# Performance work log

Measured on AMD Instinct MI355X. Metric: run time of the kernel, lower is better.

Reference implementation:

```python
import jax, jax.numpy as jnp
import numpy as np

B, T, F, D, H, L = 4, 1024, 128, 512, 8, 4
DFF = 4 * D
NE, MD = 16, 20
HD = D // H
SCALE = 1.0 / HD ** 0.5


def _ln(x, w, b):
    m = jnp.mean(x, axis=-1, keepdims=True)
    v = jnp.mean((x - m) ** 2, axis=-1, keepdims=True)
    return (x - m) * jax.lax.rsqrt(v + 1e-5) * w + b


def setup_inputs() -> dict:
    key = jax.random.key(0)
    ks = jax.random.split(key, 16)
    rn = lambda k, shape: jax.random.normal(k, shape, jnp.float32) * 0.02
    return {
        'node_features': jax.random.normal(ks[0], (B, T, F), jnp.float32),
        'centrality': jax.random.uniform(ks[1], (B, T), jnp.float32),
        'edge_types': jax.random.randint(ks[2], (B, T, T), 0, NE),
        'sp_dist': jax.random.randint(ks[3], (B, T, T), 0, MD + 1),
        'node_W': rn(ks[4], (F, D)), 'node_b': jnp.zeros((D,), jnp.float32),
        'cent_W': rn(ks[5], (D,)), 'cent_b': jnp.zeros((D,), jnp.float32),
        'edge_emb': rn(ks[6], (NE, H)), 'dist_emb': rn(ks[7], (MD + 1, H)),
        'ln1_w': jnp.ones((L, D), jnp.float32), 'ln1_b': jnp.zeros((L, D), jnp.float32),
        'q_W': rn(ks[8], (L, D, D)), 'q_b': jnp.zeros((L, D), jnp.float32),
        'k_W': rn(ks[9], (L, D, D)), 'k_b': jnp.zeros((L, D), jnp.float32),
        'v_W': rn(ks[10], (L, D, D)), 'v_b': jnp.zeros((L, D), jnp.float32),
        'o_W': rn(ks[11], (L, D, D)), 'o_b': jnp.zeros((L, D), jnp.float32),
        'ln2_w': jnp.ones((L, D), jnp.float32), 'ln2_b': jnp.zeros((L, D), jnp.float32),
        'f1_W': rn(ks[12], (L, D, DFF)), 'f1_b': jnp.zeros((L, DFF), jnp.float32),
        'f2_W': rn(ks[13], (L, DFF, D)), 'f2_b': jnp.zeros((L, D), jnp.float32),
    }


def _forward(node_features, centrality, edge_types, sp_dist,
             node_W, node_b, cent_W, cent_b, edge_emb, dist_emb,
             ln1_w, ln1_b, q_W, q_b, k_W, k_b, v_W, v_b, o_W, o_b,
             ln2_w, ln2_b, f1_W, f1_b, f2_W, f2_b):
    # node embedding + centrality encoding
    h = node_features @ node_W + node_b                      # [B,T,D]
    h = h + centrality[..., None] * cent_W + cent_b          # Linear(1,D)
    # Graphormer attention bias: [B,T,T,H] -> [B,H,T,T]
    sp = jnp.clip(sp_dist, 0, MD)
    attn_bias = (edge_emb[edge_types] + dist_emb[sp]).transpose(0, 3, 1, 2)

    def step(h, p):
        l1w, l1b, qW, qb, kW, kb, vW, vb, oW, ob, l2w, l2b, w1, b1, w2, b2 = p
        x = _ln(h, l1w, l1b)
        q = (x @ qW + qb).reshape(B, T, H, HD)
        k = (x @ kW + kb).reshape(B, T, H, HD)
        v = (x @ vW + vb).reshape(B, T, H, HD)
        scores = jnp.einsum('bihd,bjhd->bhij', q, k) * SCALE + attn_bias
        attn = jax.nn.softmax(scores, axis=-1)
        o = jnp.einsum('bhij,bjhd->bihd', attn, v).reshape(B, T, D)
        h = h + (o @ oW + ob)                                # dropout in eval mode
        x2 = _ln(h, l2w, l2b)
        h = h + (jax.nn.silu(x2 @ w1 + b1) @ w2 + b2)
        return h, None

    layer_params = (ln1_w, ln1_b, q_W, q_b, k_W, k_b, v_W, v_b, o_W, o_b,
                    ln2_w, ln2_b, f1_W, f1_b, f2_W, f2_b)
    h, _ = jax.lax.scan(step, h, layer_params)
    return h


def reference(node_features, centrality, edge_types, sp_dist,
              node_W, node_b, cent_W, cent_b, edge_emb, dist_emb,
              ln1_w, ln1_b, q_W, q_b, k_W, k_b, v_W, v_b, o_W, o_b,
              ln2_w, ln2_b, f1_W, f1_b, f2_W, f2_b):
    return _forward(node_features, centrality, edge_types, sp_dist,
                    node_W, node_b, cent_W, cent_b, edge_emb, dist_emb,
                    ln1_w, ln1_b, q_W, q_b, k_W, k_b, v_W, v_b, o_W, o_b,
                    ln2_w, ln2_b, f1_W, f1_b, f2_W, f2_b)
```

## Files before the change

### kernel.cpp

```cpp
#include <hip/hip_runtime.h>
#include <cstddef>
#include <cstdint>

#define B_    4
#define T_    1024
#define F_    128
#define D_    512
#define H_    8
#define L_    4
#define DFF_  2048
#define HD_   64
#define SCALE_ 0.125f
#define LOG2E_ 1.4426950408889634f
#define CL2E_  (SCALE_ * LOG2E_)

typedef __attribute__((ext_vector_type(8))) short bf16x8;
typedef __attribute__((ext_vector_type(4))) float f32x4;

#define AS1(p) ((const __attribute__((address_space(1))) void*)(p))
#define AS3(p) ((__attribute__((address_space(3))) void*)(p))

__device__ __forceinline__ short f2bf(float f) {
    unsigned u = __float_as_uint(f);
    u += 0x7FFFu + ((u >> 16) & 1u);
    return (short)(u >> 16);
}
__device__ __forceinline__ float bf2f(short s) {
    return __uint_as_float(((unsigned)(unsigned short)s) << 16);
}

#define PIPE_BARRIER(rem, W2, W1)                                             \
    if ((rem) >= 2)      asm volatile("s_waitcnt vmcnt(" #W2 ")" ::: "memory"); \
    else if ((rem) == 1) asm volatile("s_waitcnt vmcnt(" #W1 ")" ::: "memory"); \
    else                 asm volatile("s_waitcnt vmcnt(0)"      ::: "memory"); \
    __builtin_amdgcn_s_barrier();                                             \
    __builtin_amdgcn_sched_barrier(0);

template <int NP>
__global__ __launch_bounds__(256) void ln_k(
    float* __restrict__ X, const float* __restrict__ P0,
    const float* __restrict__ P1, const float* __restrict__ w,
    const float* __restrict__ b, short* __restrict__ Y)
{
    const int row = blockIdx.x;
    const int tid = threadIdx.x;
    float* xr = X + (size_t)row * D_;
    float v0 = xr[tid];
    float v1 = xr[tid + 256];
    if (NP == 2) {
        const size_t o0 = (size_t)row * D_ + tid;
        const size_t o1 = o0 + 256;
        v0 += P0[o0] + P1[o0];
        v1 += P0[o1] + P1[o1];
        xr[tid]       = v0;
        xr[tid + 256] = v1;
    }
    float s  = v0 + v1;
    float s2 = v0 * v0 + v1 * v1;
#pragma unroll
    for (int off = 1; off < 64; off <<= 1) {
        s  += __shfl_xor(s,  off);
        s2 += __shfl_xor(s2, off);
    }
    __shared__ float ss[4], ss2[4];
    if ((tid & 63) == 0) { ss[tid >> 6] = s; ss2[tid >> 6] = s2; }
    __syncthreads();
    s  = ss[0]  + ss[1]  + ss[2]  + ss[3];
    s2 = ss2[0] + ss2[1] + ss2[2] + ss2[3];
    const float mean = s * (1.f / D_);
    const float var  = s2 * (1.f / D_) - mean * mean;
    const float r    = rsqrtf(var + 1e-5f);
    short* yr = Y + (size_t)row * D_;
    yr[tid]       = f2bf((v0 - mean) * r * w[tid]       + b[tid]);
    yr[tid + 256] = f2bf((v1 - mean) * r * w[tid + 256] + b[tid + 256]);
}

__global__ __launch_bounds__(256) void red_k(
    const float* __restrict__ X, const float* __restrict__ P0,
    const float* __restrict__ P1, float* __restrict__ Dst)
{
    const int i = (blockIdx.x * 256 + threadIdx.x) << 2;
    const float4 a = *(const float4*)(X + i);
    const float4 p = *(const float4*)(P0 + i);
    const float4 q = *(const float4*)(P1 + i);
    *(float4*)(Dst + i) = make_float4(a.x + p.x + q.x, a.y + p.y + q.y,
                                      a.z + p.z + q.z, a.w + p.w + q.w);
}

__global__ __launch_bounds__(256) void setup_k(
    const float* __restrict__ qW, const float* __restrict__ kW,
    const float* __restrict__ vW, const float* __restrict__ oW,
    const float* __restrict__ f1W, const float* __restrict__ f2W,
    const float* __restrict__ nW,
    short* __restrict__ WqkvT, short* __restrict__ WoT,
    short* __restrict__ Wf1T, short* __restrict__ Wf2T,
    short* __restrict__ nWt,
    const int* __restrict__ et, const int* __restrict__ sp,
    const float* __restrict__ ee, const float* __restrict__ de,
    unsigned char* __restrict__ biasT8,
    const float* __restrict__ nf, short* __restrict__ nfb,
    const float* __restrict__ qb, const float* __restrict__ kb,
    const float* __restrict__ vb, float* __restrict__ biasf)
{
    const int bid = blockIdx.x;
    const int tid = threadIdx.x;

    if (bid < 12352) {
        const float* src; short* dst; int K, N, nt, tile;
        if (bid < 3072) {
            const int mat = bid >> 8;  tile = bid & 255;
            const int l = mat / 3, which = mat % 3;
            const float* s3 = (which == 0) ? qW : (which == 1) ? kW : vW;
            src = s3 + (size_t)l * D_ * D_;
            dst = WqkvT + (size_t)mat * D_ * D_;
            K = D_; N = D_; nt = 16;
        } else if (bid < 4096) {
            const int mat = (bid - 3072) >> 8;  tile = (bid - 3072) & 255;
            src = oW + (size_t)mat * D_ * D_;  dst = WoT + (size_t)mat * D_ * D_;
            K = D_; N = D_; nt = 16;
        } else if (bid < 8192) {
            const int mat = (bid - 4096) >> 10; tile = (bid - 4096) & 1023;
            src = f1W + (size_t)mat * D_ * DFF_; dst = Wf1T + (size_t)mat * DFF_ * D_;
            K = D_; N = DFF_; nt = 64;
        } else if (bid < 12288) {
            const int mat = (bid - 8192) >> 10; tile = (bid - 8192) & 1023;
            src = f2W + (size_t)mat * DFF_ * D_; dst = Wf2T + (size_t)mat * D_ * DFF_;
            K = DFF_; N = D_; nt = 16;
        } else {
            tile = bid - 12288;
            src = nW; dst = nWt; K = F_; N = D_; nt = 16;
        }
        const int k0 = (tile / nt) << 5, n0 = (tile % nt) << 5;
        __shared__ float t[32][33];
        const int c = tid & 31, r0 = tid >> 5;
#pragma unroll
        for (int i = 0; i < 32; i += 8)
            t[r0 + i][c] = src[(size_t)(k0 + r0 + i) * N + n0 + c];
        __syncthreads();
#pragma unroll
        for (int i = 0; i < 32; i += 8)
            dst[(size_t)(n0 + r0 + i) * K + k0 + c] = f2bf(t[c][r0 + i]);
        return;
    }

    const int pb = bid - 12352;
    if (pb >= 4096) {
        if (pb < 4608) {
            const int i = (((pb - 4096) << 8) + tid) << 2;
            const float4 v = *(const float4*)(nf + i);
            *(short4*)(nfb + i) =
                make_short4(f2bf(v.x), f2bf(v.y), f2bf(v.z), f2bf(v.w));
        } else {
            const int i = ((pb - 4608) << 8) + tid;
            const int l = i / 1536, c = i % 1536;
            float v;
            if (c < 512)       v = qb[l * 512 + c];
            else if (c < 1024) v = kb[l * 512 + c - 512];
            else               v = vb[l * 512 + c - 1024];
            biasf[i] = v;
        }
        return;
    }
    __shared__ float eeS[16][9], deS[21][9];
    if (tid < 128) eeS[tid >> 3][tid & 7] = ee[tid];
    for (int t2 = tid; t2 < 168; t2 += 256)
        deS[t2 >> 3][t2 & 7] = de[t2];
    __syncthreads();
    const int gid = pb * 256 + tid;
    const int j4  = (gid & 255) << 2;
    const int bi  = gid >> 8;
    const size_t base = (size_t)bi * T_ + j4;
    const int4 e = *(const int4*)(et + base);
    const int4 s = *(const int4*)(sp + base);
    const int b = bi >> 10, i = bi & 1023;
    const int ex[4] = {e.x, e.y, e.z, e.w};
    const int sx[4] = {min(s.x, 20), min(s.y, 20), min(s.z, 20), min(s.w, 20)};
#pragma unroll
    for (int h = 0; h < 8; ++h) {
        uchar4 o;
        float v;
        v = (eeS[ex[0]][h] + deS[sx[0]][h]) * LOG2E_ + 0.5f;
        o.x = (unsigned char)(int)fminf(fmaxf(v * 255.f + 0.5f, 0.f), 255.f);
        v = (eeS[ex[1]][h] + deS[sx[1]][h]) * LOG2E_ + 0.5f;
        o.y = (unsigned char)(int)fminf(fmaxf(v * 255.f + 0.5f, 0.f), 255.f);
        v = (eeS[ex[2]][h] + deS[sx[2]][h]) * LOG2E_ + 0.5f;
        o.z = (unsigned char)(int)fminf(fmaxf(v * 255.f + 0.5f, 0.f), 255.f);
        v = (eeS[ex[3]][h] + deS[sx[3]][h]) * LOG2E_ + 0.5f;
        o.w = (unsigned char)(int)fminf(fmaxf(v * 255.f + 0.5f, 0.f), 255.f);
        *(uchar4*)(biasT8 + ((size_t)((b * H_ + h) * T_ + i)) * T_ + j4) = o;
    }
}

__global__ __launch_bounds__(256) void embed_mm_k(
    const short* __restrict__ A, const short* __restrict__ Wt,
    const float* __restrict__ nb, const float* __restrict__ cb,
    const float* __restrict__ cW, const float* __restrict__ cent,
    float* __restrict__ C)
{
    const int K = F_, N = D_;
    __shared__ short As[4][128 * 32];
    __shared__ short Bs[4][64 * 32];
    const int tid  = threadIdx.x;
    const int lane = tid & 63, wv = tid >> 6;
    const int lb = blockIdx.x;
    const int xcd = lb & 7, jj = lb >> 3;
    const int bx = jj & 7, by = (xcd << 2) + (jj >> 3);
    const int bm = by << 7, bn = bx << 6;
    const int wm = (wv & 1) << 6, wn = (wv >> 1) << 5;

    const int c0 = (wv << 6) + lane;
    const int m0 = c0 >> 2, q0 = (c0 & 3) ^ ((m0 >> 1) & 3);
    const int c1 = 256 + c0;
    const int m1 = c1 >> 2, q1 = (c1 & 3) ^ ((m1 >> 1) & 3);

    const short* gA0 = A  + (size_t)(bm + m0) * K + (q0 << 3);
    const short* gA1 = A  + (size_t)(bm + m1) * K + (q1 << 3);
    const short* gB0 = Wt + (size_t)(bn + m0) * K + (q0 << 3);

    f32x4 acc[4][2];
#pragma unroll
    for (int i = 0; i < 4; ++i)
#pragma unroll
        for (int j = 0; j < 2; ++j)
            acc[i][j] = (f32x4){0.f, 0.f, 0.f, 0.f};

    const int fm = lane & 15, fq = lane >> 4;
    int caddr[4], baddr[2];
#pragma unroll
    for (int t = 0; t < 4; ++t) {
        const int rowA = wm + (t << 4) + fm;
        caddr[t] = ((rowA << 2) + (fq ^ ((rowA >> 1) & 3))) << 3;
    }
#pragma unroll
    for (int t = 0; t < 2; ++t) {
        const int rowB = wn + (t << 4) + fm;
        baddr[t] = ((rowB << 2) + (fq ^ ((rowB >> 1) & 3))) << 3;
    }

#define EMB_STAGE(KK, BUF) do { \
    __builtin_amdgcn_global_load_lds(AS1(gA0 + (KK)), AS3(&As[BUF][(wv << 9)]),        16, 0, 0); \
    __builtin_amdgcn_global_load_lds(AS1(gA1 + (KK)), AS3(&As[BUF][2048 + (wv << 9)]), 16, 0, 0); \
    __builtin_amdgcn_global_load_lds(AS1(gB0 + (KK)), AS3(&Bs[BUF][(wv << 9)]),        16, 0, 0); \
} while (0)

    EMB_STAGE(0, 0); EMB_STAGE(32, 1); EMB_STAGE(64, 2);
    const int nt = K >> 5;
    for (int t = 0; t < nt; ++t) {
        const int rem = nt - 1 - t;
        PIPE_BARRIER(rem, 6, 3);
        if (rem >= 3) EMB_STAGE((t + 3) << 5, (t + 3) & 3);
        const short* Asc = As[t & 3];
        const short* Bsc = Bs[t & 3];
        bf16x8 af[4], bf[2];
#pragma unroll
        for (int u = 0; u < 4; ++u) af[u] = *(const bf16x8*)(Asc + caddr[u]);
#pragma unroll
        for (int u = 0; u < 2; ++u) bf[u] = *(const bf16x8*)(Bsc + baddr[u]);
#pragma unroll
        for (int i = 0; i < 4; ++i)
#pragma unroll
            for (int j = 0; j < 2; ++j)
                acc[i][j] = __builtin_amdgcn_mfma_f32_16x16x32_bf16(
                    af[i], bf[j], acc[i][j], 0, 0, 0);
    }
#undef EMB_STAGE

    const int col0 = bn + wn + fm;
    const int row0 = bm + wm + (fq << 2);
#pragma unroll
    for (int j = 0; j < 2; ++j) {
        const int colg = col0 + (j << 4);
        const float bb = nb[colg] + cb[colg];
        const float cw = cW[colg];
#pragma unroll
        for (int i = 0; i < 4; ++i) {
#pragma unroll
            for (int r = 0; r < 4; ++r) {
                const int rowg = row0 + (i << 4) + r;
                C[(size_t)rowg * N + colg] = acc[i][j][r] + bb + cent[rowg] * cw;
            }
        }
    }
}

template <int OUTM, int ACT, int RES>
__global__ __launch_bounds__(256) void mm_k(
    const short* __restrict__ A, const short* __restrict__ Wt,
    const float* __restrict__ bias, const float* __restrict__ R,
    void* __restrict__ Cv, int M, int N, int K)
{
    __shared__ short As[4][128 * 32];
    __shared__ short Bs[4][128 * 32];
    const int tid  = threadIdx.x;
    const int lane = tid & 63, wv = tid >> 6;
    const int lb = blockIdx.x;
    const int xcd = lb & 7, jj = lb >> 3;
    const int bx = jj & 15, by = (xcd << 2) + (jj >> 4);
    const int bm = by << 7, bn = bx << 7;
    const int wm = (wv & 1) << 6, wn = (wv >> 1) << 6;

    const int c0 = (wv << 6) + lane;
    const int m0 = c0 >> 2, q0 = (c0 & 3) ^ ((m0 >> 1) & 3);
    const int c1 = 256 + c0;
    const int m1 = c1 >> 2, q1 = (c1 & 3) ^ ((m1 >> 1) & 3);

    const short* gA0 = A  + (size_t)(bm + m0) * K + (q0 << 3);
    const short* gA1 = A  + (size_t)(bm + m1) * K + (q1 << 3);
    const short* gB0 = Wt + (size_t)(bn + m0) * K + (q0 << 3);
    const short* gB1 = Wt + (size_t)(bn + m1) * K + (q1 << 3);

    f32x4 acc[4][4];
#pragma unroll
    for (int i = 0; i < 4; ++i)
#pragma unroll
        for (int j = 0; j < 4; ++j)
            acc[i][j] = (f32x4){0.f, 0.f, 0.f, 0.f};

    const int fm = lane & 15, fq = lane >> 4;
    int caddr[4], baddr[4];
#pragma unroll
    for (int t = 0; t < 4; ++t) {
        const int rowA = wm + (t << 4) + fm;
        caddr[t] = ((rowA << 2) + (fq ^ ((rowA >> 1) & 3))) << 3;
        const int rowB = wn + (t << 4) + fm;
        baddr[t] = ((rowB << 2) + (fq ^ ((rowB >> 1) & 3))) << 3;
    }

#define MM_STAGE(KK, BUF) do { \
    __builtin_amdgcn_global_load_lds(AS1(gA0 + (KK)), AS3(&As[BUF][(wv << 9)]),        16, 0, 0); \
    __builtin_amdgcn_global_load_lds(AS1(gA1 + (KK)), AS3(&As[BUF][2048 + (wv << 9)]), 16, 0, 0); \
    __builtin_amdgcn_global_load_lds(AS1(gB0 + (KK)), AS3(&Bs[BUF][(wv << 9)]),        16, 0, 0); \
    __builtin_amdgcn_global_load_lds(AS1(gB1 + (KK)), AS3(&Bs[BUF][2048 + (wv << 9)]), 16, 0, 0); \
} while (0)

    MM_STAGE(0, 0); MM_STAGE(32, 1); MM_STAGE(64, 2);
    const int nt = K >> 5;
    for (int t = 0; t < nt; ++t) {
        const int rem = nt - 1 - t;
        PIPE_BARRIER(rem, 8, 4);
        if (rem >= 3) MM_STAGE((t + 3) << 5, (t + 3) & 3);
        const short* Asc = As[t & 3];
        const short* Bsc = Bs[t & 3];
        bf16x8 af[4], bf[4];
#pragma unroll
        for (int u = 0; u < 4; ++u) {
            af[u] = *(const bf16x8*)(Asc + caddr[u]);
            bf[u] = *(const bf16x8*)(Bsc + baddr[u]);
        }
#pragma unroll
        for (int i = 0; i < 4; ++i)
#pragma unroll
            for (int j = 0; j < 4; ++j)
                acc[i][j] = __builtin_amdgcn_mfma_f32_16x16x32_bf16(
                    af[i], bf[j], acc[i][j], 0, 0, 0);
    }
#undef MM_STAGE

    const int col0 = bn + wn + fm;
    const int row0 = bm + wm + (fq << 2);
    float* Cf = (float*)Cv;
    short* Cb = (short*)Cv;
#pragma unroll
    for (int j = 0; j < 4; ++j) {
        const int colg = col0 + (j << 4);
        const float bb = bias[colg];
#pragma unroll
        for (int i = 0; i < 4; ++i) {
#pragma unroll
            for (int r = 0; r < 4; ++r) {
                const int rowg = row0 + (i << 4) + r;
                float v = acc[i][j][r] + bb;
                if (ACT) v = v / (1.f + __expf(-v));
                const size_t off = (size_t)rowg * N + colg;
                if (RES) v += R[off];
                if (OUTM == 1) Cb[off] = f2bf(v);
                else           Cf[off] = v;
            }
        }
    }
}

__global__ __launch_bounds__(256) void qkv64_k(
    const short* __restrict__ A, const short* __restrict__ Wt,
    const float* __restrict__ bias, short* __restrict__ QKb,
    short* __restrict__ VtOut)
{
    const int K = D_;
    __shared__ short As[4][128 * 32];
    __shared__ short Bs[4][64 * 32];
    const int tid  = threadIdx.x;
    const int lane = tid & 63, wv = tid >> 6;
    const int lb = blockIdx.x;
    const int xcd = lb & 7, jj = lb >> 3;
    const int yl = jj / 24, bx = jj - yl * 24;
    const int by = (xcd << 2) + yl;
    const int bm = by << 7, bn = bx << 6;
    const int wm = (wv & 1) << 6, wn = (wv >> 1) << 5;

    const int c0 = (wv << 6) + lane;
    const int m0 = c0 >> 2, q0 = (c0 & 3) ^ ((m0 >> 1) & 3);
    const int c1 = 256 + c0;
    const int m1 = c1 >> 2, q1 = (c1 & 3) ^ ((m1 >> 1) & 3);

    const short* gA0 = A  + (size_t)(bm + m0) * K + (q0 << 3);
    const short* gA1 = A  + (size_t)(bm + m1) * K + (q1 << 3);
    const short* gB0 = Wt + (size_t)(bn + m0) * K + (q0 << 3);

    f32x4 acc[4][2];
#pragma unroll
    for (int i = 0; i < 4; ++i)
#pragma unroll
        for (int j = 0; j < 2; ++j)
            acc[i][j] = (f32x4){0.f, 0.f, 0.f, 0.f};

    const int fm = lane & 15, fq = lane >> 4;
    int caddr[4], baddr[2];
#pragma unroll
    for (int t = 0; t < 4; ++t) {
        const int rowA = wm + (t << 4) + fm;
        caddr[t] = ((rowA << 2) + (fq ^ ((rowA >> 1) & 3))) << 3;
    }
#pragma unroll
    for (int t = 0; t < 2; ++t) {
        const int rowB = wn + (t << 4) + fm;
        baddr[t] = ((rowB << 2) + (fq ^ ((rowB >> 1) & 3))) << 3;
    }

#define QKV_STAGE(KK, BUF) do { \
    __builtin_amdgcn_global_load_lds(AS1(gA0 + (KK)), AS3(&As[BUF][(wv << 9)]),        16, 0, 0); \
    __builtin_amdgcn_global_load_lds(AS1(gA1 + (KK)), AS3(&As[BUF][2048 + (wv << 9)]), 16, 0, 0); \
    __builtin_amdgcn_global_load_lds(AS1(gB0 + (KK)), AS3(&Bs[BUF][(wv << 9)]),        16, 0, 0); \
} while (0)

    QKV_STAGE(0, 0); QKV_STAGE(32, 1); QKV_STAGE(64, 2);
    const int nt = K >> 5;
    for (int t = 0; t < nt; ++t) {
        const int rem = nt - 1 - t;
        PIPE_BARRIER(rem, 6, 3);
        if (rem >= 3) QKV_STAGE((t + 3) << 5, (t + 3) & 3);
        const short* Asc = As[t & 3];
        const short* Bsc = Bs[t & 3];
        bf16x8 af[4], bf[2];
#pragma unroll
        for (int u = 0; u < 4; ++u) af[u] = *(const bf16x8*)(Asc + caddr[u]);
#pragma unroll
        for (int u = 0; u < 2; ++u) bf[u] = *(const bf16x8*)(Bsc + baddr[u]);
#pragma unroll
        for (int i = 0; i < 4; ++i)
#pragma unroll
            for (int j = 0; j < 2; ++j)
                acc[i][j] = __builtin_amdgcn_mfma_f32_16x16x32_bf16(
                    af[i], bf[j], acc[i][j], 0, 0, 0);
    }
#undef QKV_STAGE

    const int col0 = bn + wn + fm;
    const int row0 = bm + wm + (fq << 2);
#pragma unroll
    for (int j = 0; j < 2; ++j) {
        const int colg = col0 + (j << 4);
        const float bb = bias[colg];
#pragma unroll
        for (int i = 0; i < 4; ++i) {
#pragma unroll
            for (int r = 0; r < 4; ++r) {
                const int rowg = row0 + (i << 4) + r;
                const float v = acc[i][j][r] + bb;
                if (colg < 1024) {
                    QKb[(size_t)rowg * 1024 + colg] = f2bf(v);
                } else {
                    const int da = colg - 1024;
                    const int hh = da >> 6, dd = da & 63;
                    const int bb2 = rowg >> 10, tt = rowg & 1023;
                    VtOut[((size_t)(bb2 * H_ + hh) * 64 + dd) * T_ + tt] = f2bf(v);
                }
            }
        }
    }
}

__global__ __launch_bounds__(256) void flash_k(
    const short* __restrict__ QKb, const short* __restrict__ Vt,
    const unsigned char* __restrict__ biasT8, short* __restrict__ OpartB,
    float* __restrict__ Lpart)
{
    const int tid = threadIdx.x;
    const int bx = blockIdx.x;
    const int it = bx >> 1, split = bx & 1;
    const int i0 = it << 6;
    const int h  = blockIdx.y;
    const int b  = blockIdx.z;
    const int lane = tid & 63, w = tid >> 6;
    const int fm = lane & 15, q = lane >> 4;

    __shared__ short Ks[4096];
    __shared__ short Vs[4096];
    __shared__ unsigned char Bsh8[4096];
    __shared__ short Ps[64][72];

    const short* qp = QKb + (size_t)(b * T_ + i0 + (w << 4) + fm) * 1024 + (h << 6) + (q << 3);
    const bf16x8 aq0 = *(const bf16x8*)(qp);
    const bf16x8 aq1 = *(const bf16x8*)(qp + 32);

    const int s0 = (w << 6) + lane, r0 = s0 >> 3, cc0 = (s0 & 7) ^ (r0 & 7);
    const int s1 = 256 + s0,        r1 = s1 >> 3, cc1 = (s1 & 7) ^ (r1 & 7);
    const short* gK0 = QKb + (size_t)(b * T_ + r0) * 1024 + 512 + (h << 6) + (cc0 << 3);
    const short* gK1 = QKb + (size_t)(b * T_ + r1) * 1024 + 512 + (h << 6) + (cc1 << 3);
    const short* gV0 = Vt + ((size_t)((b * H_ + h) << 6) + r0) * T_ + (cc0 << 3);
    const short* gV1 = Vt + ((size_t)((b * H_ + h) << 6) + r1) * T_ + (cc1 << 3);
    const int br = s0 >> 2, bc = (s0 & 3) ^ (br & 3);
    const unsigned char* gB0 = biasT8 +
        ((size_t)(b * H_ + h) * T_ + i0 + br) * T_ + (bc << 4);

    int fAddr[4][2];
#pragma unroll
    for (int t = 0; t < 4; ++t) {
        const int row = (t << 4) + fm;
#pragma unroll
        for (int ks = 0; ks < 2; ++ks)
            fAddr[t][ks] = (row << 6) + (((q + (ks << 2)) ^ (row & 7)) << 3);
    }

    int bAddr[4][4];
#pragma unroll
    for (int r = 0; r < 4; ++r) {
        const int rowL = (w << 4) + (q << 2) + r;
#pragma unroll
        for (int jt = 0; jt < 4; ++jt)
            bAddr[r][jt] = (rowL << 6) + (((jt ^ (rowL & 3))) << 4) + fm;
    }

    const short oneb = 0x3F80;
    const bf16x8 ones = {oneb, oneb, oneb, oneb, oneb, oneb, oneb, oneb};

    f32x4 accO[4];
#pragma unroll
    for (int dt = 0; dt < 4; ++dt) accO[dt] = (f32x4){0.f, 0.f, 0.f, 0.f};
    f32x4 accL = (f32x4){0.f, 0.f, 0.f, 0.f};

    const int irow = b * T_ + i0 + (w << 4) + (q << 2);
    short* psW = &Ps[(w << 4) + (q << 2)][fm];
    const short* psR = &Ps[(w << 4) + fm][q << 3];

    const int jbeg = split << 9, jend = jbeg + 512;
    for (int j0 = jbeg; j0 < jend; j0 += 64) {
        __syncthreads();
        __builtin_amdgcn_global_load_lds(AS1(gK0 + (size_t)j0 * 1024), AS3(Ks + (s0 << 3)), 16, 0, 0);
        __builtin_amdgcn_global_load_lds(AS1(gK1 + (size_t)j0 * 1024), AS3(Ks + (s1 << 3)), 16, 0, 0);
        __builtin_amdgcn_global_load_lds(AS1(gV0 + j0), AS3(Vs + (s0 << 3)), 16, 0, 0);
        __builtin_amdgcn_global_load_lds(AS1(gV1 + j0), AS3(Vs + (s1 << 3)), 16, 0, 0);
        __builtin_amdgcn_global_load_lds(AS1(gB0 + j0), AS3(Bsh8 + (s0 << 4)), 16, 0, 0);
        __syncthreads();

        f32x4 s[4];
#pragma unroll
        for (int jt = 0; jt < 4; ++jt) s[jt] = (f32x4){0.f, 0.f, 0.f, 0.f};
        __builtin_amdgcn_s_setprio(1);
#pragma unroll
        for (int jt = 0; jt < 4; ++jt) {
            const bf16x8 k0 = *(const bf16x8*)(Ks + fAddr[jt][0]);
            const bf16x8 k1 = *(const bf16x8*)(Ks + fAddr[jt][1]);
            s[jt] = __builtin_amdgcn_mfma_f32_16x16x32_bf16(aq0, k0, s[jt], 0, 0, 0);
            s[jt] = __builtin_amdgcn_mfma_f32_16x16x32_bf16(aq1, k1, s[jt], 0, 0, 0);
        }
        __builtin_amdgcn_s_setprio(0);

#pragma unroll
        for (int r = 0; r < 4; ++r)
#pragma unroll
            for (int jt = 0; jt < 4; ++jt) {
                const float q8 = (float)Bsh8[bAddr[r][jt]];
                const float bb = fmaf(q8, 1.f / 255.f, -0.5f);
                const float p = __builtin_amdgcn_exp2f(fmaf(s[jt][r], CL2E_, bb));
                psW[(size_t)r * 72 + (jt << 4)] = f2bf(p);
            }

        __builtin_amdgcn_s_setprio(1);
#pragma unroll
        for (int ks = 0; ks < 2; ++ks) {
            const bf16x8 ap = *(const bf16x8*)(psR + (ks << 5));
            accL = __builtin_amdgcn_mfma_f32_16x16x32_bf16(ap, ones, accL, 0, 0, 0);
#pragma unroll
            for (int dt = 0; dt < 4; ++dt) {
                const bf16x8 bv = *(const bf16x8*)(Vs + fAddr[dt][ks]);
                accO[dt] = __builtin_amdgcn_mfma_f32_16x16x32_bf16(ap, bv, accO[dt], 0, 0, 0);
            }
        }
        __builtin_amdgcn_s_setprio(0);
    }

    short* obase = OpartB + (size_t)split * B_ * T_ * D_;
#pragma unroll
    for (int r = 0; r < 4; ++r) {
        short* op = obase + (size_t)(irow + r) * D_ + (h << 6) + fm;
#pragma unroll
        for (int dt = 0; dt < 4; ++dt)
            op[dt << 4] = f2bf(accO[dt][r]);
    }
    if (fm == 0) {
#pragma unroll
        for (int r = 0; r < 4; ++r)
            Lpart[(size_t)split * B_ * T_ * H_ + (size_t)(irow + r) * H_ + h] = accL[r];
    }
}

__global__ __launch_bounds__(256) void combine_k(
    const short* __restrict__ OpartB, const float* __restrict__ Lpart,
    short* __restrict__ Ob)
{
    const int gid = blockIdx.x * 256 + threadIdx.x;
    const int d4  = (gid & 127) << 2;
    const int row = gid >> 7;
    const int h   = d4 >> 6;
    const float l = Lpart[(size_t)row * H_ + h] +
                    Lpart[(size_t)B_ * T_ * H_ + (size_t)row * H_ + h];
    const float inv = 1.f / l;
    const size_t o = (size_t)row * D_ + d4;
    const short4 a = *(const short4*)(OpartB + o);
    const short4 c = *(const short4*)(OpartB + (size_t)B_ * T_ * D_ + o);
    short4 r = make_short4(
        f2bf((bf2f(a.x) + bf2f(c.x)) * inv), f2bf((bf2f(a.y) + bf2f(c.y)) * inv),
        f2bf((bf2f(a.z) + bf2f(c.z)) * inv), f2bf((bf2f(a.w) + bf2f(c.w)) * inv));
    *(short4*)(Ob + o) = r;
}

__global__ __launch_bounds__(256) void mm64p_k(
    const short* __restrict__ A, const short* __restrict__ Wt,
    const float* __restrict__ bias, float* __restrict__ P,
    int M, int N, int K, int KS)
{
    __shared__ short As[4][128 * 32];
    __shared__ short Bs[4][64 * 32];
    const int tid  = threadIdx.x;
    const int lane = tid & 63, wv = tid >> 6;
    const int lb = blockIdx.x;
    const int xcd = lb & 7, jj = lb >> 3;
    const int z  = jj >> 5;
    const int jr = jj & 31;
    const int bx = jr & 7, by = (xcd << 2) + (jr >> 3);
    const int bm = by << 7, bn = bx << 6;
    const int ks0 = z * KS;
    const int wm = (wv & 1) << 6, wn = (wv >> 1) << 5;

    const int c0 = (wv << 6) + lane;
    const int m0 = c0 >> 2, q0 = (c0 & 3) ^ ((m0 >> 1) & 3);
    const int c1 = 256 + c0;
    const int m1 = c1 >> 2, q1 = (c1 & 3) ^ ((m1 >> 1) & 3);

    const short* gA0 = A  + (size_t)(bm + m0) * K + ks0 + (q0 << 3);
    const short* gA1 = A  + (size_t)(bm + m1) * K + ks0 + (q1 << 3);
    const short* gB0 = Wt + (size_t)(bn + m0) * K + ks0 + (q0 << 3);

    f32x4 acc[4][2];
#pragma unroll
    for (int i = 0; i < 4; ++i)
#pragma unroll
        for (int j = 0; j < 2; ++j)
            acc[i][j] = (f32x4){0.f, 0.f, 0.f, 0.f};

    const int fm = lane & 15, fq = lane >> 4;
    int caddr[4], baddr[2];
#pragma unroll
    for (int t = 0; t < 4; ++t) {
        const int rowA = wm + (t << 4) + fm;
        caddr[t] = ((rowA << 2) + (fq ^ ((rowA >> 1) & 3))) << 3;
    }
#pragma unroll
    for (int t = 0; t < 2; ++t) {
        const int rowB = wn + (t << 4) + fm;
        baddr[t] = ((rowB << 2) + (fq ^ ((rowB >> 1) & 3))) << 3;
    }

#define MM64_STAGE(KK, BUF) do { \
    __builtin_amdgcn_global_load_lds(AS1(gA0 + (KK)), AS3(&As[BUF][(wv << 9)]),        16, 0, 0); \
    __builtin_amdgcn_global_load_lds(AS1(gA1 + (KK)), AS3(&As[BUF][2048 + (wv << 9)]), 16, 0, 0); \
    __builtin_amdgcn_global_load_lds(AS1(gB0 + (KK)), AS3(&Bs[BUF][(wv << 9)]),        16, 0, 0); \
} while (0)

    MM64_STAGE(0, 0); MM64_STAGE(32, 1); MM64_STAGE(64, 2);
    const int nt = KS >> 5;
    for (int t = 0; t < nt; ++t) {
        const int rem = nt - 1 - t;
        PIPE_BARRIER(rem, 6, 3);
        if (rem >= 3) MM64_STAGE((t + 3) << 5, (t + 3) & 3);
        const short* Asc = As[t & 3];
        const short* Bsc = Bs[t & 3];
        bf16x8 af[4], bf[2];
#pragma unroll
        for (int u = 0; u < 4; ++u) af[u] = *(const bf16x8*)(Asc + caddr[u]);
#pragma unroll
        for (int u = 0; u < 2; ++u) bf[u] = *(const bf16x8*)(Bsc + baddr[u]);
#pragma unroll
        for (int i = 0; i < 4; ++i)
#pragma unroll
            for (int j = 0; j < 2; ++j)
                acc[i][j] = __builtin_amdgcn_mfma_f32_16x16x32_bf16(
                    af[i], bf[j], acc[i][j], 0, 0, 0);
    }
#undef MM64_STAGE

    const int col0 = bn + wn + fm;
    const int row0 = bm + wm + (fq << 2);
    float* Pz = P + (size_t)z * M * N;
#pragma unroll
    for (int j = 0; j < 2; ++j) {
        const int colg = col0 + (j << 4);
        const float bb = (z == 0) ? bias[colg] : 0.f;
#pragma unroll
        for (int i = 0; i < 4; ++i) {
#pragma unroll
            for (int r = 0; r < 4; ++r) {
                const int rowg = row0 + (i << 4) + r;
                Pz[(size_t)rowg * N + colg] = acc[i][j][r] + bb;
            }
        }
    }
}

extern "C" void kernel_launch(void* const* d_in, const int* in_sizes, int n_in,
                              void* d_out, int out_size, void* d_ws, size_t ws_size,
                              hipStream_t stream)
{
    (void)in_sizes; (void)n_in; (void)out_size; (void)ws_size;

    const float* nf   = (const float*)d_in[0];
    const float* cent = (const float*)d_in[1];
    const int*   et   = (const int*)  d_in[2];
    const int*   sp   = (const int*)  d_in[3];
    const float* nW   = (const float*)d_in[4];
    const float* nb   = (const float*)d_in[5];
    const float* cW   = (const float*)d_in[6];
    const float* cb   = (const float*)d_in[7];
    const float* ee   = (const float*)d_in[8];
    const float* de   = (const float*)d_in[9];
    const float* ln1w = (const float*)d_in[10];
    const float* ln1b = (const float*)d_in[11];
    const float* qW   = (const float*)d_in[12];
    const float* qb   = (const float*)d_in[13];
    const float* kW   = (const float*)d_in[14];
    const float* kb   = (const float*)d_in[15];
    const float* vW   = (const float*)d_in[16];
    const float* vb   = (const float*)d_in[17];
    const float* oW   = (const float*)d_in[18];
    const float* ob   = (const float*)d_in[19];
    const float* ln2w = (const float*)d_in[20];
    const float* ln2b = (const float*)d_in[21];
    const float* f1W  = (const float*)d_in[22];
    const float* f1b  = (const float*)d_in[23];
    const float* f2W  = (const float*)d_in[24];
    const float* f2b  = (const float*)d_in[25];

    const int M = B_ * T_;
    char* p = (char*)d_ws;
    float* Hbuf  = (float*)p;  p += (size_t)M * D_ * 4;
    short* QKb   = (short*)p;  p += (size_t)M * 1024 * 2;
    short* Vt    = (short*)p;  p += (size_t)B_ * H_ * 64 * T_ * 2;
    float* biasf = (float*)p;  p += (size_t)L_ * 3 * D_ * 4;
    short* Xbuf  = (short*)p;  p += (size_t)M * D_ * 2;
    short* Ob    = (short*)p;  p += (size_t)M * D_ * 2;
    short* FF    = (short*)p;  p += (size_t)M * DFF_ * 2;
    unsigned char* biasT8 = (unsigned char*)p; p += (size_t)B_ * H_ * T_ * T_;
    short* WqkvT = (short*)p;  p += (size_t)L_ * 3 * D_ * D_ * 2;
    short* WoT   = (short*)p;  p += (size_t)L_ * D_ * D_ * 2;
    short* Wf1T  = (short*)p;  p += (size_t)L_ * DFF_ * D_ * 2;
    short* Wf2T  = (short*)p;  p += (size_t)L_ * D_ * DFF_ * 2;
    short* nfb   = (short*)p;  p += (size_t)M * F_ * 2;
    short* nWt   = (short*)p;  p += (size_t)D_ * F_ * 2;
    short* OpartB = (short*)p; p += (size_t)2 * M * D_ * 2;
    float* Lpart = (float*)p;  p += (size_t)2 * M * H_ * 4;
    float* Pbuf  = (float*)p;  p += (size_t)2 * M * D_ * 4;

    float* out = (float*)d_out;

    setup_k<<<dim3(16984), dim3(256), 0, stream>>>(
        qW, kW, vW, oW, f1W, f2W, nW, WqkvT, WoT, Wf1T, Wf2T, nWt,
        et, sp, ee, de, biasT8, nf, nfb, qb, kb, vb, biasf);
    embed_mm_k<<<dim3(256), dim3(256), 0, stream>>>(
        nfb, nWt, nb, cb, cW, cent, Hbuf);

    const dim3 blk(256);
    const dim3 gQKV(768);
    const dim3 gO64p(512);
    const dim3 gF1 (512);
    const dim3 gAttn(2 * T_ / 64, H_, B_);
    const dim3 gCmb(M * D_ / 1024);

    for (int l = 0; l < L_; ++l) {
        const size_t bOff  = (size_t)l * D_;
        const size_t b1Off = (size_t)l * DFF_;

        if (l == 0)
            ln_k<0><<<dim3(M), blk, 0, stream>>>(
                Hbuf, nullptr, nullptr, ln1w + bOff, ln1b + bOff, Xbuf);
        else
            ln_k<2><<<dim3(M), blk, 0, stream>>>(
                Hbuf, Pbuf, Pbuf + (size_t)M * D_, ln1w + bOff, ln1b + bOff, Xbuf);

        qkv64_k<<<gQKV, blk, 0, stream>>>(
            Xbuf, WqkvT + (size_t)l * 3 * D_ * D_, biasf + (size_t)l * 3 * D_,
            QKb, Vt);

        flash_k<<<gAttn, blk, 0, stream>>>(QKb, Vt, biasT8, OpartB, Lpart);
        combine_k<<<gCmb, blk, 0, stream>>>(OpartB, Lpart, Ob);

        mm64p_k<<<gO64p, blk, 0, stream>>>(
            Ob, WoT + (size_t)l * D_ * D_, ob + bOff, Pbuf, M, D_, D_, D_ / 2);

        ln_k<2><<<dim3(M), blk, 0, stream>>>(
            Hbuf, Pbuf, Pbuf + (size_t)M * D_, ln2w + bOff, ln2b + bOff, Xbuf);

        mm_k<1, 1, 0><<<gF1, blk, 0, stream>>>(
            Xbuf, Wf1T + (size_t)l * DFF_ * D_, f1b + b1Off, nullptr, FF, M, DFF_, D_);

        mm64p_k<<<gO64p, blk, 0, stream>>>(
            FF, Wf2T + (size_t)l * D_ * DFF_, f2b + bOff, Pbuf, M, D_, DFF_, DFF_ / 2);
    }

    red_k<<<gCmb, blk, 0, stream>>>(Hbuf, Pbuf, Pbuf + (size_t)M * D_, out);
}
```

Measured before the change: 633.6 us.

## Drop split-KV in flash attention and normalize output in-kernel, removing combine pass

The attention kernel no longer splits the key range into two halves. Each block now loops over all 1024 keys and writes the normalized output directly, so the combine kernel and its partial-output and partial-sum buffers are gone. This removes one launch per layer and the round trip of the partial results through memory, at the cost of half as many attention blocks (512 instead of 1024) and a longer serial loop per block. The s_setprio hints around the MFMA sections are also removed.

```diff
diff --git a/kernel.cpp b/kernel.cpp
--- a/kernel.cpp
+++ b/kernel.cpp
@@ -481,13 +481,10 @@
 
 __global__ __launch_bounds__(256) void flash_k(
     const short* __restrict__ QKb, const short* __restrict__ Vt,
-    const unsigned char* __restrict__ biasT8, short* __restrict__ OpartB,
-    float* __restrict__ Lpart)
+    const unsigned char* __restrict__ biasT8, short* __restrict__ Ob)
 {
     const int tid = threadIdx.x;
-    const int bx = blockIdx.x;
-    const int it = bx >> 1, split = bx & 1;
-    const int i0 = it << 6;
+    const int i0 = blockIdx.x << 6;
     const int h  = blockIdx.y;
     const int b  = blockIdx.z;
     const int lane = tid & 63, w = tid >> 6;
@@ -542,8 +539,7 @@
     short* psW = &Ps[(w << 4) + (q << 2)][fm];
     const short* psR = &Ps[(w << 4) + fm][q << 3];
 
-    const int jbeg = split << 9, jend = jbeg + 512;
-    for (int j0 = jbeg; j0 < jend; j0 += 64) {
+    for (int j0 = 0; j0 < T_; j0 += 64) {
         __syncthreads();
         __builtin_amdgcn_global_load_lds(AS1(gK0 + (size_t)j0 * 1024), AS3(Ks + (s0 << 3)), 16, 0, 0);
         __builtin_amdgcn_global_load_lds(AS1(gK1 + (size_t)j0 * 1024), AS3(Ks + (s1 << 3)), 16, 0, 0);
@@ -555,7 +551,6 @@
         f32x4 s[4];
 #pragma unroll
         for (int jt = 0; jt < 4; ++jt) s[jt] = (f32x4){0.f, 0.f, 0.f, 0.f};
-        __builtin_amdgcn_s_setprio(1);
 #pragma unroll
         for (int jt = 0; jt < 4; ++jt) {
             const bf16x8 k0 = *(const bf16x8*)(Ks + fAddr[jt][0]);
@@ -563,7 +558,6 @@
             s[jt] = __builtin_amdgcn_mfma_f32_16x16x32_bf16(aq0, k0, s[jt], 0, 0, 0);
             s[jt] = __builtin_amdgcn_mfma_f32_16x16x32_bf16(aq1, k1, s[jt], 0, 0, 0);
         }
-        __builtin_amdgcn_s_setprio(0);
 
 #pragma unroll
         for (int r = 0; r < 4; ++r)
@@ -575,7 +569,6 @@
                 psW[(size_t)r * 72 + (jt << 4)] = f2bf(p);
             }
 
-        __builtin_amdgcn_s_setprio(1);
 #pragma unroll
         for (int ks = 0; ks < 2; ++ks) {
             const bf16x8 ap = *(const bf16x8*)(psR + (ks << 5));
@@ -586,42 +579,16 @@
                 accO[dt] = __builtin_amdgcn_mfma_f32_16x16x32_bf16(ap, bv, accO[dt], 0, 0, 0);
             }
         }
-        __builtin_amdgcn_s_setprio(0);
-    }
-
-    short* obase = OpartB + (size_t)split * B_ * T_ * D_;
+    }
+
 #pragma unroll
     for (int r = 0; r < 4; ++r) {
-        short* op = obase + (size_t)(irow + r) * D_ + (h << 6) + fm;
+        const float inv = 1.f / accL[r];
+        short* op = Ob + (size_t)(irow + r) * D_ + (h << 6) + fm;
 #pragma unroll
         for (int dt = 0; dt < 4; ++dt)
-            op[dt << 4] = f2bf(accO[dt][r]);
-    }
-    if (fm == 0) {
-#pragma unroll
-        for (int r = 0; r < 4; ++r)
-            Lpart[(size_t)split * B_ * T_ * H_ + (size_t)(irow + r) * H_ + h] = accL[r];
-    }
-}
-
-__global__ __launch_bounds__(256) void combine_k(
-    const short* __restrict__ OpartB, const float* __restrict__ Lpart,
-    short* __restrict__ Ob)
-{
-    const int gid = blockIdx.x * 256 + threadIdx.x;
-    const int d4  = (gid & 127) << 2;
-    const int row = gid >> 7;
-    const int h   = d4 >> 6;
-    const float l = Lpart[(size_t)row * H_ + h] +
-                    Lpart[(size_t)B_ * T_ * H_ + (size_t)row * H_ + h];
-    const float inv = 1.f / l;
-    const size_t o = (size_t)row * D_ + d4;
-    const short4 a = *(const short4*)(OpartB + o);
-    const short4 c = *(const short4*)(OpartB + (size_t)B_ * T_ * D_ + o);
-    short4 r = make_short4(
-        f2bf((bf2f(a.x) + bf2f(c.x)) * inv), f2bf((bf2f(a.y) + bf2f(c.y)) * inv),
-        f2bf((bf2f(a.z) + bf2f(c.z)) * inv), f2bf((bf2f(a.w) + bf2f(c.w)) * inv));
-    *(short4*)(Ob + o) = r;
+            op[dt << 4] = f2bf(accO[dt][r] * inv);
+    }
 }
 
 __global__ __launch_bounds__(256) void mm64p_k(
@@ -766,8 +733,6 @@
     short* Wf2T  = (short*)p;  p += (size_t)L_ * D_ * DFF_ * 2;
     short* nfb   = (short*)p;  p += (size_t)M * F_ * 2;
     short* nWt   = (short*)p;  p += (size_t)D_ * F_ * 2;
-    short* OpartB = (short*)p; p += (size_t)2 * M * D_ * 2;
-    float* Lpart = (float*)p;  p += (size_t)2 * M * H_ * 4;
     float* Pbuf  = (float*)p;  p += (size_t)2 * M * D_ * 4;
 
     float* out = (float*)d_out;
@@ -782,7 +747,7 @@
     const dim3 gQKV(768);
     const dim3 gO64p(512);
     const dim3 gF1 (512);
-    const dim3 gAttn(2 * T_ / 64, H_, B_);
+    const dim3 gAttn(T_ / 64, H_, B_);
     const dim3 gCmb(M * D_ / 1024);
 
     for (int l = 0; l < L_; ++l) {
@@ -800,8 +765,7 @@
             Xbuf, WqkvT + (size_t)l * 3 * D_ * D_, biasf + (size_t)l * 3 * D_,
             QKb, Vt);
 
-        flash_k<<<gAttn, blk, 0, stream>>>(QKb, Vt, biasT8, OpartB, Lpart);
-        combine_k<<<gCmb, blk, 0, stream>>>(OpartB, Lpart, Ob);
+        flash_k<<<gAttn, blk, 0, stream>>>(QKb, Vt, biasT8, Ob);
 
         mm64p_k<<<gO64p, blk, 0, stream>>>(
             Ob, WoT + (size_t)l * D_ * D_, ob + bOff, Pbuf, M, D_, D_, D_ / 2);
```

Result: no change. 628.5 us (-0.8%).
